# Performance work log

Measured on AMD Instinct MI355X. Metric: run time of the kernel, lower is better.

Reference implementation:

```python
import jax, jax.numpy as jnp
import numpy as np

B, QS, KS, E, H = 2, 2048, 2048, 2048, 16
D = E // H  # head_dim = 128
EPS = 1e-6


def setup_inputs() -> dict:
    key = jax.random.key(0)
    ks = jax.random.split(key, 11)
    scale_in = 1.0 / np.sqrt(E)  # lecun_normal fan_in = E
    scale_out = 1.0 / np.sqrt(E)  # fan_in for out proj = H*D = E
    return {
        "q": jax.random.normal(ks[0], (B, QS, E), jnp.float32),
        "kv": jax.random.normal(ks[1], (B, KS, E), jnp.float32),
        "q_pos": jax.random.normal(ks[2], (B, QS, E), jnp.float32),
        "kv_pos": jax.random.normal(ks[3], (B, KS, E), jnp.float32),
        "mask": jax.random.bernoulli(ks[4], 0.5, (B, QS, KS)),
        "wq": jax.random.normal(ks[5], (E, H, D), jnp.float32) * scale_in,
        "wk": jax.random.normal(ks[6], (E, H, D), jnp.float32) * scale_in,
        "wv": jax.random.normal(ks[7], (E, H, D), jnp.float32) * scale_in,
        "q_ln_scale": jnp.ones((D,), jnp.float32),
        "k_ln_scale": jnp.ones((D,), jnp.float32),
        "wo": jax.random.normal(ks[8], (H, D, E), jnp.float32) * scale_out,
    }


def _layernorm_no_bias(x, scale):
    # flax LayerNorm over last axis, use_bias=False, epsilon=1e-6
    mu = jnp.mean(x, axis=-1, keepdims=True)
    var = jnp.mean(jnp.square(x - mu), axis=-1, keepdims=True)
    return (x - mu) * jax.lax.rsqrt(var + EPS) * scale


def reference(q, kv, q_pos, kv_pos, mask, wq, wk, wv, q_ln_scale, k_ln_scale, wo):
    dtype = q.dtype
    qi = q + q_pos          # [b, qs, e]
    ki = kv + kv_pos        # [b, ks, e]
    vi = kv
    # QKV projections (DenseGeneral, no bias) -> [b, s, h, d]
    qh = jnp.einsum('bqe,ehd->bqhd', qi, wq)
    kh = jnp.einsum('bke,ehd->bkhd', ki, wk)
    vh = jnp.einsum('bke,ehd->bkhd', vi, wv)
    # normalize_qk: LayerNorm (no bias) on query/key over head_dim
    qh = _layernorm_no_bias(qh, q_ln_scale)
    kh = _layernorm_no_bias(kh, k_ln_scale)
    # scaled dot-product with float32 logits
    qh = qh / jnp.sqrt(jnp.asarray(D, dtype))
    logits = jnp.einsum('bqhd,bkhd->bhqk', qh, kh,
                        preferred_element_type=jnp.float32)
    big_neg = jnp.finfo(jnp.float32).min
    logits = jnp.where(mask[:, None, :, :], logits, big_neg)
    attn = jax.nn.softmax(logits, axis=-1).astype(dtype)  # [b,h,q,k]
    out = jnp.einsum('bhqk,bkhd->bqhd', attn, vh)
    # output projection (DenseGeneral over (h,d), no bias)
    return jnp.einsum('bqhd,hde->bqe', out, wo)
```

## Files before the change

### kernel.cpp

```cpp
#include <hip/hip_runtime.h>
#include <hip/hip_bf16.h>


typedef __attribute__((ext_vector_type(8))) __bf16 bf16x8;
typedef __attribute__((ext_vector_type(4))) float f32x4;
typedef __attribute__((ext_vector_type(16))) float f32x16;
typedef __attribute__((ext_vector_type(8))) unsigned short ushort8;
typedef __attribute__((ext_vector_type(4))) unsigned short ushort4v;
typedef __attribute__((ext_vector_type(4))) unsigned uint4v;
typedef __attribute__((ext_vector_type(4))) float float4v;

#define MFMA16(a, b, c) __builtin_amdgcn_mfma_f32_16x16x32_bf16((a), (b), (c), 0, 0, 0)
#define MFMA32(a, b, c) __builtin_amdgcn_mfma_f32_32x32x16_bf16((a), (b), (c), 0, 0, 0)

__device__ __forceinline__ unsigned short f2bf(float f) {
  unsigned u = __builtin_bit_cast(unsigned, f);
  u += 0x7fffu + ((u >> 16) & 1u);
  return (unsigned short)(u >> 16);
}

__device__ __forceinline__ unsigned pkbf(float lo, float hi) {
  unsigned d;
  asm("v_cvt_pk_bf16_f32 %0, %1, %2" : "=v"(d) : "v"(lo), "v"(hi));
  return d;
}

__device__ __forceinline__ float max3f(float a, float b, float c) {
  float d;
  asm("v_max3_f32 %0, %1, %2, %3" : "=v"(d) : "v"(a), "v"(b), "v"(c));
  return d;
}

__device__ __forceinline__ float exp2a(float x) {
  float d;
  asm("v_exp_f32 %0, %1" : "=v"(d) : "v"(x));
  return d;
}

__device__ __forceinline__ void gload_lds16(const void* g, void* l) {
  __builtin_amdgcn_global_load_lds(
      (const __attribute__((address_space(1))) void*)g,
      (__attribute__((address_space(3))) void*)l, 16, 0, 0);
}

__global__ __launch_bounds__(256) void k_cvt(const float4v* __restrict__ x,
                                             const float4v* __restrict__ y,
                                             ushort4v* __restrict__ o, int n4) {
  int i = blockIdx.x * 256 + threadIdx.x;
  if (i >= n4) return;
  float4v a = x[i];
  if (y) { float4v b = y[i]; a = a + b; }
  ushort4v r;
  r[0] = f2bf(a[0]); r[1] = f2bf(a[1]); r[2] = f2bf(a[2]); r[3] = f2bf(a[3]);
  o[i] = r;
}

__global__ __launch_bounds__(256) void k_cvt2(const float4v* __restrict__ x,
                                              const float4v* __restrict__ y,
                                              ushort4v* __restrict__ oa,
                                              ushort4v* __restrict__ ob, int n4) {
  int i = blockIdx.x * 256 + threadIdx.x;
  if (i >= n4) return;
  float4v a = x[i];
  float4v s = a + y[i];
  ushort4v ra, rb;
  ra[0] = f2bf(s[0]); ra[1] = f2bf(s[1]); ra[2] = f2bf(s[2]); ra[3] = f2bf(s[3]);
  rb[0] = f2bf(a[0]); rb[1] = f2bf(a[1]); rb[2] = f2bf(a[2]); rb[3] = f2bf(a[3]);
  oa[i] = ra; ob[i] = rb;
}

__global__ __launch_bounds__(256) void k_tr(const float* __restrict__ s0, const float* __restrict__ s1,
                                            const float* __restrict__ s2, const float* __restrict__ s3,
                                            unsigned short* __restrict__ d0, unsigned short* __restrict__ d1,
                                            unsigned short* __restrict__ d2, unsigned short* __restrict__ d3) {
  __shared__ float t[32][33];
  const float* S; unsigned short* D;
  switch (blockIdx.z) {
    case 0: S = s0; D = d0; break;
    case 1: S = s1; D = d1; break;
    case 2: S = s2; D = d2; break;
    default: S = s3; D = d3; break;
  }
  int x = threadIdx.x & 31, y = threadIdx.x >> 5;
  int r0 = blockIdx.y * 32, c0 = blockIdx.x * 32;
#pragma unroll
  for (int i = 0; i < 4; ++i) t[y + 8 * i][x] = S[(size_t)(r0 + y + 8 * i) * 2048 + c0 + x];
  __syncthreads();
#pragma unroll
  for (int i = 0; i < 4; ++i)
    D[(size_t)(c0 + y + 8 * i) * 2048 + r0 + x] = f2bf(t[x][y + 8 * i]);
}

__global__ __launch_bounds__(256) void k_mask(const int* __restrict__ m,
                                              unsigned long long* __restrict__ out) {
  int i = blockIdx.x * 256 + threadIdx.x;
  unsigned long long b = __ballot(m[i] != 0);
  if ((threadIdx.x & 63) == 0) out[i >> 6] = b;
}

template <int MODE>
__global__ __launch_bounds__(512, 2) void k_gemm8(const unsigned short* __restrict__ A,
                                                  const unsigned short* __restrict__ Bt,
                                                  void* __restrict__ Cv,
                                                  const float* __restrict__ lnsc) {
  constexpr int K = 2048;
  constexpr int NT = 32;
  constexpr int BUF = 49152;
  __shared__ __attribute__((aligned(16))) char smem[3 * BUF];
  int tid = threadIdx.x;
  int lane = tid & 63, w = tid >> 6;
  int wr = w >> 2, wc = w & 3;
  int r15 = lane & 15, blk = lane >> 4;
  int n0 = blockIdx.x * 128, m0 = blockIdx.y * 256;
  const unsigned short* Abase = A + (size_t)m0 * K;
  const unsigned short* Bbase = Bt + (size_t)n0 * K;
  f32x4 acc[8][2] = {};

  const unsigned short* ag[4]; int al[4];
  const unsigned short* bg[2]; int bl[2];
#pragma unroll
  for (int i = 0; i < 4; ++i) {
    int c = i * 512 + tid;
    int row = c >> 3, cc = c & 7;
    ag[i] = Abase + (size_t)row * K + ((cc ^ (row & 7)) * 8);
    al[i] = c * 16;
  }
#pragma unroll
  for (int i = 0; i < 2; ++i) {
    int c = i * 512 + tid;
    int row = c >> 3, cc = c & 7;
    bg[i] = Bbase + (size_t)row * K + ((cc ^ (row & 7)) * 8);
    bl[i] = 32768 + c * 16;
  }

  auto stage = [&](int t) {
    char* buf = smem + (t % 3) * BUF;
    int kt = t * 64;
#pragma unroll
    for (int i = 0; i < 4; ++i) gload_lds16(ag[i] + kt, buf + al[i]);
#pragma unroll
    for (int i = 0; i < 2; ++i) gload_lds16(bg[i] + kt, buf + bl[i]);
  };

  stage(0);
  stage(1);

  for (int t = 0; t < NT; ++t) {
    if (t + 2 < NT) {
      stage(t + 2);
      asm volatile("s_waitcnt vmcnt(6)" ::: "memory");
    } else {
      asm volatile("s_waitcnt vmcnt(0)" ::: "memory");
    }
    __builtin_amdgcn_s_barrier();
    __builtin_amdgcn_sched_barrier(0);
    const unsigned short* sA = (const unsigned short*)(smem + (t % 3) * BUF);
    const unsigned short* sB = (const unsigned short*)(smem + (t % 3) * BUF + 32768);
#pragma unroll
    for (int kk = 0; kk < 2; ++kk) {
      bf16x8 av[8], bv[2];
#pragma unroll
      for (int i = 0; i < 8; ++i) {
        int row = wr * 128 + i * 16 + r15;
        av[i] = *(const bf16x8*)&sA[row * 64 + (((kk * 4 + blk) ^ (row & 7)) * 8)];
      }
#pragma unroll
      for (int j = 0; j < 2; ++j) {
        int row = wc * 32 + j * 16 + r15;
        bv[j] = *(const bf16x8*)&sB[row * 64 + (((kk * 4 + blk) ^ (row & 7)) * 8)];
      }
#pragma unroll
      for (int i = 0; i < 8; ++i)
#pragma unroll
        for (int j = 0; j < 2; ++j) acc[i][j] = MFMA16(av[i], bv[j], acc[i][j]);
    }
    asm volatile("s_waitcnt lgkmcnt(0)" ::: "memory");
    __builtin_amdgcn_s_barrier();
  }
  __syncthreads();

  if constexpr (MODE == 3) {
    float* C = (float*)Cv;
#pragma unroll
    for (int i = 0; i < 8; ++i)
#pragma unroll
      for (int r = 0; r < 4; ++r) {
        int rowl = wr * 128 + i * 16 + blk * 4 + r;
#pragma unroll
        for (int j = 0; j < 2; ++j) {
          int coll = wc * 32 + j * 16 + r15;
          C[(size_t)(m0 + rowl) * 2048 + n0 + coll] = acc[i][j][r];
        }
      }
  } else if constexpr (MODE == 4) {
    unsigned short* Vtp = (unsigned short*)Cv;
    int p15 = (r15 & 3) | ((r15 & 4) << 1) | ((r15 & 8) >> 1);
#pragma unroll
    for (int i = 0; i < 8; ++i)
#pragma unroll
      for (int r = 0; r < 4; ++r) {
        int rowg = m0 + wr * 128 + i * 16 + blk * 4 + r;
        int h = rowg >> 7, d = rowg & 127;
#pragma unroll
        for (int j = 0; j < 2; ++j) {
          int col = n0 + wc * 32 + j * 16;
          int b = col >> 11, s16 = col & 2047;
          Vtp[(((size_t)(b * 16 + h) * 128 + d) * 2048) + s16 + p15] = f2bf(acc[i][j][r]);
        }
      }
  } else {
    float* sSum = (float*)smem;
    float* sSq  = (float*)smem + 1024;
#pragma unroll
    for (int i = 0; i < 8; ++i)
#pragma unroll
      for (int r = 0; r < 4; ++r) {
        float v0 = acc[i][0][r], v1 = acc[i][1][r];
        float sm = v0 + v1, sq = v0 * v0 + v1 * v1;
        sm += __shfl_xor(sm, 1); sq += __shfl_xor(sq, 1);
        sm += __shfl_xor(sm, 2); sq += __shfl_xor(sq, 2);
        sm += __shfl_xor(sm, 4); sq += __shfl_xor(sq, 4);
        sm += __shfl_xor(sm, 8); sq += __shfl_xor(sq, 8);
        if (r15 == 0) {
          int rowl = wr * 128 + i * 16 + blk * 4 + r;
          sSum[wc * 256 + rowl] = sm;
          sSq[wc * 256 + rowl] = sq;
        }
      }
    __syncthreads();
    unsigned short* Hout = (unsigned short*)Cv;
    int h = blockIdx.x;
#pragma unroll
    for (int i = 0; i < 8; ++i)
#pragma unroll
      for (int r = 0; r < 4; ++r) {
        int rowl = wr * 128 + i * 16 + blk * 4 + r;
        float sm = (sSum[rowl] + sSum[256 + rowl]) + (sSum[512 + rowl] + sSum[768 + rowl]);
        float sq = (sSq[rowl] + sSq[256 + rowl]) + (sSq[512 + rowl] + sSq[768 + rowl]);
        float mean = sm * 0.0078125f;
        float var = sq * 0.0078125f - mean * mean;
        float rstd = rsqrtf(var + 1e-6f);
        int rowg = m0 + rowl;
        int b = rowg >> 11, s = rowg & 2047;
        unsigned short* orow = Hout + (((size_t)b * 16 + h) * 2048 + s) * 128;
#pragma unroll
        for (int j = 0; j < 2; ++j) {
          int d = wc * 32 + j * 16 + r15;
          float v = acc[i][j][r];
          if constexpr (MODE == 1)
            v = (v - mean) * rstd * lnsc[d] * (0.08838834764831845f * 1.4426950408889634f);
          else
            v = (v - mean) * rstd * lnsc[d];
          orow[d] = f2bf(v);
        }
      }
  }
}

__global__ __launch_bounds__(256, 2) void k_attn(const unsigned short* __restrict__ Qh,
                                                 const unsigned short* __restrict__ Kh,
                                                 const unsigned short* __restrict__ Vtp,
                                                 const unsigned* __restrict__ maskb,
                                                 unsigned short* __restrict__ O) {
  __shared__ __attribute__((aligned(16))) char smem[65536];
  int tid = threadIdx.x, w = tid >> 6;
  int lane = tid & 63;
  int q31 = lane & 31, hi = lane >> 5;
  int bh = blockIdx.y, b = bh >> 4, h = bh & 15;
  int qb = blockIdx.x * 128;
  size_t base = (size_t)bh * (2048 * 128);
  int qrow = qb + w * 32 + q31;

  bf16x8 qf[8];
  {
    const unsigned short* qp = Qh + base + (size_t)qrow * 128 + hi * 8;
#pragma unroll
    for (int wd = 0; wd < 8; ++wd) qf[wd] = *(const bf16x8*)(qp + wd * 16);
  }
  const unsigned* mrow = maskb + ((size_t)b * 2048 + qrow) * 64;

  const unsigned short* kgp[4];
  const unsigned short* vgp[4];
#pragma unroll
  for (int i = 0; i < 4; ++i) {
    int c = i * 256 + tid;
    int rr = c >> 4, cc = c & 15;
    kgp[i] = Kh + base + (size_t)rr * 128 + ((cc ^ (rr & 15)) * 8);
    int d = c >> 3, c8 = c & 7;
    vgp[i] = Vtp + base + (size_t)d * 2048 + ((c8 ^ (d & 7)) * 8);
  }

  f32x16 o[4] = {};
  float mv = -1e30f, ls = 0.f;

#pragma unroll
  for (int i = 0; i < 4; ++i) {
    int c = i * 256 + tid;
    gload_lds16(kgp[i], smem + c * 16);
    gload_lds16(vgp[i], smem + 16384 + c * 16);
  }
  __syncthreads();

  int cur = 0;
  for (int kc = 0; kc < 2048; kc += 64) {
    if (kc + 64 < 2048) {
      char* nb = smem + ((cur ^ 1) << 15);
#pragma unroll
      for (int i = 0; i < 4; ++i) {
        int c = i * 256 + tid;
        gload_lds16(kgp[i] + (size_t)(kc + 64) * 128, nb + c * 16);
        gload_lds16(vgp[i] + (kc + 64), nb + 16384 + c * 16);
      }
    }
    const unsigned short* sK = (const unsigned short*)(smem + (cur << 15));
    const unsigned short* sV = (const unsigned short*)(smem + (cur << 15) + 16384);

    unsigned mw0 = mrow[kc >> 5] >> (4 * hi);
    unsigned mw1 = mrow[(kc >> 5) + 1] >> (4 * hi);

    f32x16 st0 = {}, st1 = {};
    __builtin_amdgcn_s_setprio(1);
#pragma unroll
    for (int wd = 0; wd < 8; ++wd) {
      int ck = ((2 * wd + hi) ^ (q31 & 15)) * 8;
      bf16x8 k0 = *(const bf16x8*)&sK[q31 * 128 + ck];
      bf16x8 k1 = *(const bf16x8*)&sK[(32 + q31) * 128 + ck];
      st0 = MFMA32(k0, qf[wd], st0);
      st1 = MFMA32(k1, qf[wd], st1);
    }
    __builtin_amdgcn_s_setprio(0);

    float pvv[32];
#pragma unroll
    for (int r = 0; r < 16; ++r) {
      int bit = (r & 3) + 8 * (r >> 2);
      pvv[r] = ((mw0 >> bit) & 1u) ? st0[r] : -1e30f;
      pvv[16 + r] = ((mw1 >> bit) & 1u) ? st1[r] : -1e30f;
    }
    float c0 = max3f(pvv[0], pvv[1], pvv[2]);
    float c1 = max3f(pvv[3], pvv[4], pvv[5]);
    float c2 = max3f(pvv[6], pvv[7], pvv[8]);
    float c3 = max3f(pvv[9], pvv[10], pvv[11]);
    float c4 = max3f(pvv[12], pvv[13], pvv[14]);
    float c5 = max3f(pvv[15], pvv[16], pvv[17]);
    float c6 = max3f(pvv[18], pvv[19], pvv[20]);
    float c7 = max3f(pvv[21], pvv[22], pvv[23]);
    float c8 = max3f(pvv[24], pvv[25], pvv[26]);
    float c9 = max3f(pvv[27], pvv[28], pvv[29]);
    float ca = fmaxf(pvv[30], pvv[31]);
    float t0 = max3f(c0, c1, c2);
    float t1 = max3f(c3, c4, c5);
    float t2 = max3f(c6, c7, c8);
    float t3 = max3f(c9, ca, t0);
    float cmax = max3f(t1, t2, t3);
    cmax = fmaxf(cmax, __shfl_xor(cmax, 32));

    if (!__all(cmax - mv <= 11.5f)) {
      float mnew = fmaxf(mv, cmax);
      float fac = exp2a(mv - mnew);
      ls *= fac;
      float fr[16];
#pragma unroll
      for (int r = 0; r < 16; ++r) fr[r] = __shfl(fac, (r & 3) + 8 * (r >> 2) + 4 * hi);
#pragma unroll
      for (int dt = 0; dt < 4; ++dt)
#pragma unroll
        for (int r = 0; r < 16; ++r) o[dt][r] *= fr[r];
      mv = mnew;
    }

#pragma unroll
    for (int t = 0; t < 32; ++t) pvv[t] = exp2a(pvv[t] - mv);
    {
      float s0 = 0.f, s1 = 0.f, s2 = 0.f, s3 = 0.f;
#pragma unroll
      for (int t = 0; t < 8; ++t) {
        s0 += pvv[t]; s1 += pvv[8 + t]; s2 += pvv[16 + t]; s3 += pvv[24 + t];
      }
      ls += (s0 + s1) + (s2 + s3);
    }

    bf16x8 pa[4];
#pragma unroll
    for (int kw = 0; kw < 4; ++kw) {
      uint4v pw;
#pragma unroll
      for (int m = 0; m < 4; ++m) pw[m] = pkbf(pvv[8 * kw + 2 * m], pvv[8 * kw + 2 * m + 1]);
      pa[kw] = __builtin_bit_cast(bf16x8, pw);
    }

    __builtin_amdgcn_s_setprio(1);
#pragma unroll
    for (int dt = 0; dt < 4; ++dt) {
      int vrow = dt * 32 + q31;
#pragma unroll
      for (int kw = 0; kw < 4; ++kw) {
        int cv = ((2 * kw + hi) ^ (q31 & 7)) * 8;
        bf16x8 vf = *(const bf16x8*)&sV[vrow * 64 + cv];
        o[dt] = MFMA32(pa[kw], vf, o[dt]);
      }
    }
    __builtin_amdgcn_s_setprio(0);
    __syncthreads();
    cur ^= 1;
  }

  ls += __shfl_xor(ls, 32);
  float inv = 1.f / ls;
  float ir[16];
#pragma unroll
  for (int r = 0; r < 16; ++r) ir[r] = __shfl(inv, (r & 3) + 8 * (r >> 2) + 4 * hi);

  float* sO = (float*)smem;
#pragma unroll
  for (int pass = 0; pass < 2; ++pass) {
    __syncthreads();
    if ((w >> 1) == pass) {
      int wl = w & 1;
#pragma unroll
      for (int dt = 0; dt < 4; ++dt)
#pragma unroll
        for (int r = 0; r < 16; ++r) {
          int qrl = wl * 32 + (r & 3) + 8 * (r >> 2) + 4 * hi;
          sO[qrl * 132 + dt * 32 + q31] = o[dt][r] * ir[r];
        }
    }
    __syncthreads();
    {
      int row = tid >> 2, d0 = (tid & 3) * 32;
      int grow = qb + pass * 64 + row;
      unsigned short* op = O + (size_t)(b * 2048 + grow) * 2048 + h * 128 + d0;
#pragma unroll
      for (int g = 0; g < 4; ++g) {
        ushort8 pk;
#pragma unroll
        for (int e = 0; e < 8; ++e) pk[e] = f2bf(sO[row * 132 + d0 + g * 8 + e]);
        *(ushort8*)(op + g * 8) = pk;
      }
    }
  }
}

extern "C" void kernel_launch(void* const* d_in, const int* in_sizes, int n_in,
                              void* d_out, int out_size, void* d_ws, size_t ws_size,
                              hipStream_t stream) {
  const float* q      = (const float*)d_in[0];
  const float* kv     = (const float*)d_in[1];
  const float* q_pos  = (const float*)d_in[2];
  const float* kv_pos = (const float*)d_in[3];
  const int*   mask   = (const int*)d_in[4];
  const float* wq     = (const float*)d_in[5];
  const float* wk     = (const float*)d_in[6];
  const float* wv     = (const float*)d_in[7];
  const float* qls    = (const float*)d_in[8];
  const float* kls    = (const float*)d_in[9];
  const float* wo     = (const float*)d_in[10];

  char* ws = (char*)d_ws;
  const size_t SZ_ACT = (size_t)4096 * 2048 * 2;
  const size_t SZ_W   = (size_t)2048 * 2048 * 2;
  unsigned short* a_q = (unsigned short*)(ws);
  unsigned short* a_k = (unsigned short*)(ws + SZ_ACT);
  unsigned short* a_v = (unsigned short*)(ws + 2 * SZ_ACT);
  unsigned short* Qh  = (unsigned short*)(ws + 3 * SZ_ACT);
  unsigned short* Kh  = (unsigned short*)(ws + 4 * SZ_ACT);
  unsigned short* wqt = (unsigned short*)(ws + 6 * SZ_ACT);
  unsigned short* wkt = (unsigned short*)(ws + 6 * SZ_ACT + SZ_W);
  unsigned short* wvt = (unsigned short*)(ws + 6 * SZ_ACT + 2 * SZ_W);
  unsigned short* wot = (unsigned short*)(ws + 6 * SZ_ACT + 3 * SZ_W);
  unsigned*       mkb = (unsigned*)(ws + 6 * SZ_ACT + 4 * SZ_W);
  unsigned short* Ob  = a_q;
  unsigned short* Vtr = (unsigned short*)(ws + 5 * SZ_ACT);

  const size_t NEED = 6 * SZ_ACT + 4 * SZ_W + (size_t)2 * 2048 * 64 * 4;
  if (ws_size < NEED) return;

  k_cvt<<<8192, 256, 0, stream>>>((const float4v*)q, (const float4v*)q_pos, (ushort4v*)a_q, 2097152);
  k_cvt2<<<8192, 256, 0, stream>>>((const float4v*)kv, (const float4v*)kv_pos,
                                   (ushort4v*)a_k, (ushort4v*)a_v, 2097152);
  k_tr<<<dim3(64, 64, 4), 256, 0, stream>>>(wq, wk, wv, wo, wqt, wkt, wvt, wot);
  k_mask<<<32768, 256, 0, stream>>>(mask, (unsigned long long*)mkb);

  k_gemm8<1><<<dim3(16, 16), 512, 0, stream>>>(a_q, wqt, Qh, qls);
  k_gemm8<2><<<dim3(16, 16), 512, 0, stream>>>(a_k, wkt, Kh, kls);
  k_gemm8<4><<<dim3(32, 8), 512, 0, stream>>>(wvt, a_v, Vtr, nullptr);

  k_attn<<<dim3(16, 32), 256, 0, stream>>>(Qh, Kh, Vtr, mkb, Ob);

  k_gemm8<3><<<dim3(16, 16), 512, 0, stream>>>(Ob, wot, d_out, nullptr);
}
```

Before: 326.1 us.

## Remap GEMM and attention blocks per XCD and fuse prep kernels

Blocks in the GEMM and attention kernels are remapped so that the tiles sharing an A row-panel or a (batch, head) pair land on the same XCD. This is meant to improve L2 reuse on the multi-die MI355X, assuming blocks are dispatched round-robin across the 8 XCDs. The separate convert and mask-packing kernels are merged into one k_prep launch to cut launch overhead. The mapping relies on that assumed round-robin dispatch order and on the fixed grid shapes.

```diff
diff --git a/kernel.cpp b/kernel.cpp
--- a/kernel.cpp
+++ b/kernel.cpp
@@ -43,30 +43,35 @@
       (__attribute__((address_space(3))) void*)l, 16, 0, 0);
 }
 
-__global__ __launch_bounds__(256) void k_cvt(const float4v* __restrict__ x,
-                                             const float4v* __restrict__ y,
-                                             ushort4v* __restrict__ o, int n4) {
-  int i = blockIdx.x * 256 + threadIdx.x;
-  if (i >= n4) return;
-  float4v a = x[i];
-  if (y) { float4v b = y[i]; a = a + b; }
-  ushort4v r;
-  r[0] = f2bf(a[0]); r[1] = f2bf(a[1]); r[2] = f2bf(a[2]); r[3] = f2bf(a[3]);
-  o[i] = r;
-}
-
-__global__ __launch_bounds__(256) void k_cvt2(const float4v* __restrict__ x,
-                                              const float4v* __restrict__ y,
-                                              ushort4v* __restrict__ oa,
-                                              ushort4v* __restrict__ ob, int n4) {
-  int i = blockIdx.x * 256 + threadIdx.x;
-  if (i >= n4) return;
-  float4v a = x[i];
-  float4v s = a + y[i];
-  ushort4v ra, rb;
-  ra[0] = f2bf(s[0]); ra[1] = f2bf(s[1]); ra[2] = f2bf(s[2]); ra[3] = f2bf(s[3]);
-  rb[0] = f2bf(a[0]); rb[1] = f2bf(a[1]); rb[2] = f2bf(a[2]); rb[3] = f2bf(a[3]);
-  oa[i] = ra; ob[i] = rb;
+__global__ __launch_bounds__(256) void k_prep(const float4v* __restrict__ q,
+                                              const float4v* __restrict__ q_pos,
+                                              const float4v* __restrict__ kv,
+                                              const float4v* __restrict__ kv_pos,
+                                              const int* __restrict__ mask,
+                                              ushort4v* __restrict__ a_q,
+                                              ushort4v* __restrict__ a_k,
+                                              ushort4v* __restrict__ a_v,
+                                              unsigned long long* __restrict__ mkb) {
+  int bx = blockIdx.x, tid = threadIdx.x;
+  if (bx < 8192) {
+    int i = bx * 256 + tid;
+    float4v a = q[i] + q_pos[i];
+    ushort4v r;
+    r[0] = f2bf(a[0]); r[1] = f2bf(a[1]); r[2] = f2bf(a[2]); r[3] = f2bf(a[3]);
+    a_q[i] = r;
+  } else if (bx < 16384) {
+    int i = (bx - 8192) * 256 + tid;
+    float4v a = kv[i];
+    float4v s = a + kv_pos[i];
+    ushort4v ra, rb;
+    ra[0] = f2bf(s[0]); ra[1] = f2bf(s[1]); ra[2] = f2bf(s[2]); ra[3] = f2bf(s[3]);
+    rb[0] = f2bf(a[0]); rb[1] = f2bf(a[1]); rb[2] = f2bf(a[2]); rb[3] = f2bf(a[3]);
+    a_k[i] = ra; a_v[i] = rb;
+  } else {
+    int i = (bx - 16384) * 256 + tid;
+    unsigned long long b = __ballot(mask[i] != 0);
+    if ((tid & 63) == 0) mkb[i >> 6] = b;
+  }
 }
 
 __global__ __launch_bounds__(256) void k_tr(const float* __restrict__ s0, const float* __restrict__ s1,
@@ -89,13 +94,6 @@
 #pragma unroll
   for (int i = 0; i < 4; ++i)
     D[(size_t)(c0 + y + 8 * i) * 2048 + r0 + x] = f2bf(t[x][y + 8 * i]);
-}
-
-__global__ __launch_bounds__(256) void k_mask(const int* __restrict__ m,
-                                              unsigned long long* __restrict__ out) {
-  int i = blockIdx.x * 256 + threadIdx.x;
-  unsigned long long b = __ballot(m[i] != 0);
-  if ((threadIdx.x & 63) == 0) out[i >> 6] = b;
 }
 
 template <int MODE>
@@ -111,7 +109,12 @@
   int lane = tid & 63, w = tid >> 6;
   int wr = w >> 2, wc = w & 3;
   int r15 = lane & 15, blk = lane >> 4;
-  int n0 = blockIdx.x * 128, m0 = blockIdx.y * 256;
+  int L = blockIdx.y * gridDim.x + blockIdx.x;
+  int xcd = L & 7, slot = L >> 3;
+  int mt, nt;
+  if constexpr (MODE == 4) { mt = xcd; nt = slot; }
+  else { mt = xcd * 2 + (slot >> 4); nt = slot & 15; }
+  int n0 = nt * 128, m0 = mt * 256;
   const unsigned short* Abase = A + (size_t)m0 * K;
   const unsigned short* Bbase = Bt + (size_t)n0 * K;
   f32x4 acc[8][2] = {};
@@ -229,7 +232,7 @@
       }
     __syncthreads();
     unsigned short* Hout = (unsigned short*)Cv;
-    int h = blockIdx.x;
+    int h = nt;
 #pragma unroll
     for (int i = 0; i < 8; ++i)
 #pragma unroll
@@ -266,8 +269,11 @@
   int tid = threadIdx.x, w = tid >> 6;
   int lane = tid & 63;
   int q31 = lane & 31, hi = lane >> 5;
-  int bh = blockIdx.y, b = bh >> 4, h = bh & 15;
-  int qb = blockIdx.x * 128;
+  int L = blockIdx.y * 16 + blockIdx.x;
+  int xcd = L & 7, slot = L >> 3;
+  int bh = xcd * 4 + (slot >> 4);
+  int qb = (slot & 15) * 128;
+  int b = bh >> 4, h = bh & 15;
   size_t base = (size_t)bh * (2048 * 128);
   int qrow = qb + w * 32 + q31;
 
@@ -475,11 +481,11 @@
   const size_t NEED = 6 * SZ_ACT + 4 * SZ_W + (size_t)2 * 2048 * 64 * 4;
   if (ws_size < NEED) return;
 
-  k_cvt<<<8192, 256, 0, stream>>>((const float4v*)q, (const float4v*)q_pos, (ushort4v*)a_q, 2097152);
-  k_cvt2<<<8192, 256, 0, stream>>>((const float4v*)kv, (const float4v*)kv_pos,
-                                   (ushort4v*)a_k, (ushort4v*)a_v, 2097152);
+  k_prep<<<49152, 256, 0, stream>>>((const float4v*)q, (const float4v*)q_pos,
+                                    (const float4v*)kv, (const float4v*)kv_pos, mask,
+                                    (ushort4v*)a_q, (ushort4v*)a_k, (ushort4v*)a_v,
+                                    (unsigned long long*)mkb);
   k_tr<<<dim3(64, 64, 4), 256, 0, stream>>>(wq, wk, wv, wo, wqt, wkt, wvt, wot);
-  k_mask<<<32768, 256, 0, stream>>>(mask, (unsigned long long*)mkb);
 
   k_gemm8<1><<<dim3(16, 16), 512, 0, stream>>>(a_q, wqt, Qh, qls);
   k_gemm8<2><<<dim3(16, 16), 512, 0, stream>>>(a_k, wkt, Kh, kls);
```

Result: faster. 316.2 us (-3.1%).
